# Optimization experiments

Measured on AMD Instinct MI355X. Metric: run time of the kernel, lower is better.

Reference implementation:

```python
import jax, jax.numpy as jnp
import numpy as np

METRIC_SCALE = 0.01  # metric = I + 0.01 * outer(p, p)


def setup_inputs() -> dict:
    key = jax.random.key(0)
    kq, kk = jax.random.split(key)
    query_points = jax.random.normal(kq, (8192, 512), dtype=jnp.float32)
    key_points = jax.random.normal(kk, (8192, 512), dtype=jnp.float32)
    return {"query_points": query_points, "key_points": key_points}


def reference(query_points, key_points):
    # diff_ij = q_i - k_j;  dist^2 under metric (I + c * p p^T) is
    # ||diff||^2 + c * (p . diff)^2 -- avoids materializing [Nq, Nk, d] diffs.
    c = METRIC_SCALE
    qq = jnp.sum(query_points * query_points, axis=-1)          # [Nq]
    kk = jnp.sum(key_points * key_points, axis=-1)              # [Nk]
    qk = jnp.einsum('qd,kd->qk', query_points, key_points)      # [Nq, Nk]
    norm2 = jnp.maximum(qq[:, None] + kk[None, :] - 2.0 * qk, 0.0)
    qdot = qq[:, None] - qk                                     # q_i . (q_i - k_j)
    kdot = qk - kk[None, :]                                     # k_j . (q_i - k_j) (sign irrelevant, squared)
    query_dist = jnp.sqrt(norm2 + c * qdot * qdot)
    key_dist = jnp.sqrt(norm2 + c * kdot * kdot)
    scores = -0.5 * (query_dist + key_dist)
    return jax.nn.softmax(scores, axis=-1)
```

## Files before the change

kernel.cpp:

```cpp
#include <hip/hip_runtime.h>
#include <stdint.h>


#define NQ 8192
#define NK 8192
#define DIM 512
#define CSCALE 0.01f

typedef float f32x4 __attribute__((ext_vector_type(4)));
typedef short s16x8 __attribute__((ext_vector_type(8)));
typedef unsigned short u16x4 __attribute__((ext_vector_type(4)));

__device__ __forceinline__ unsigned short f2bf(float x) {
  union { float f; uint32_t u; } c; c.f = x;
  uint32_t u = c.u;
  return (unsigned short)((u + 0x7fffu + ((u >> 16) & 1u)) >> 16);
}

__device__ __forceinline__ float bf2f(unsigned short h) {
  union { uint32_t u; float f; } c; c.u = ((uint32_t)h) << 16;
  return c.f;
}

__device__ __forceinline__ s16x8 pack8(f32x4 a, f32x4 b) {
  s16x8 r;
  r[0]=(short)f2bf(a.x); r[1]=(short)f2bf(a.y);
  r[2]=(short)f2bf(a.z); r[3]=(short)f2bf(a.w);
  r[4]=(short)f2bf(b.x); r[5]=(short)f2bf(b.y);
  r[6]=(short)f2bf(b.z); r[7]=(short)f2bf(b.w);
  return r;
}

#define GLOAD_LDS16(g, l)                                                      \
  __builtin_amdgcn_global_load_lds(                                            \
      (const __attribute__((address_space(1))) void*)(g),                      \
      (__attribute__((address_space(3))) void*)(l), 16, 0, 0)

__global__ __launch_bounds__(256) void prep_full_kernel(
    const float* __restrict__ q, const float* __restrict__ k,
    unsigned short* __restrict__ qbf, unsigned short* __restrict__ kbf,
    float* __restrict__ qq, float* __restrict__ kk) {
  int rowg = blockIdx.x * 4 + (threadIdx.x >> 6);
  int lane = threadIdx.x & 63;
  const float* src; unsigned short* dst; float* nrm; int row;
  if (rowg < NQ) { src = q; dst = qbf; nrm = qq; row = rowg; }
  else           { src = k; dst = kbf; nrm = kk; row = rowg - NQ; }
  const float* p = src + (size_t)row * DIM + lane * 8;
  f32x4 a = *(const f32x4*)p;
  f32x4 b = *(const f32x4*)(p + 4);
  float ss = a.x*a.x + a.y*a.y + a.z*a.z + a.w*a.w
           + b.x*b.x + b.y*b.y + b.z*b.z + b.w*b.w;
  *(s16x8*)(dst + (size_t)row * DIM + lane * 8) = pack8(a, b);
#pragma unroll
  for (int mask = 1; mask < 64; mask <<= 1) ss += __shfl_xor(ss, mask, 64);
  if (lane == 0) nrm[row] = ss;
}

__global__ __launch_bounds__(256) void prep_norms_kernel(
    const float* __restrict__ q, const float* __restrict__ k,
    float* __restrict__ qq, float* __restrict__ kk) {
  int rowg = blockIdx.x * 4 + (threadIdx.x >> 6);
  int lane = threadIdx.x & 63;
  const float* src; float* nrm; int row;
  if (rowg < NQ) { src = q; nrm = qq; row = rowg; }
  else           { src = k; nrm = kk; row = rowg - NQ; }
  const float* p = src + (size_t)row * DIM + lane * 8;
  f32x4 a = *(const f32x4*)p;
  f32x4 b = *(const f32x4*)(p + 4);
  float ss = a.x*a.x + a.y*a.y + a.z*a.z + a.w*a.w
           + b.x*b.x + b.y*b.y + b.z*b.z + b.w*b.w;
#pragma unroll
  for (int mask = 1; mask < 64; mask <<= 1) ss += __shfl_xor(ss, mask, 64);
  if (lane == 0) nrm[row] = ss;
}

__device__ __forceinline__ float score_fn(float qkv, float qqv, float kkv) {
  float n2 = fmaxf(qqv + kkv - 2.f * qkv, 0.f);
  float qd = qqv - qkv;
  float kd = qkv - kkv;
  return -0.5f * (sqrtf(n2 + CSCALE * qd * qd) +
                  sqrtf(n2 + CSCALE * kd * kd));
}

__global__ __launch_bounds__(256) void gemm_exp_kernel(
    const unsigned short* __restrict__ qbf, const unsigned short* __restrict__ kbf,
    const float* __restrict__ qq, const float* __restrict__ kk,
    unsigned short* __restrict__ E) {
  __shared__ unsigned short lA[128 * 32];
  __shared__ unsigned short lB[128 * 32];
  __shared__ alignas(16) unsigned short lT[4][16 * 80];
  const int tid = threadIdx.x;
  const int m0 = blockIdx.y * 128;
  const int n0 = blockIdx.x * 128;
  const int wave = tid >> 6, lane = tid & 63;
  const int wr = wave >> 1, wc = wave & 1;
  const int quad = lane >> 4, lcol = lane & 15;

  const unsigned short* ga = qbf + (size_t)(m0 + (tid >> 2)) * DIM + (tid & 3) * 8;
  const unsigned short* gb = kbf + (size_t)(n0 + (tid >> 2)) * DIM + (tid & 3) * 8;
  char* la0 = (char*)lA + wave * 1024;
  char* lb0 = (char*)lB + wave * 1024;

  f32x4 acc[4][4];
#pragma unroll
  for (int mi = 0; mi < 4; ++mi)
#pragma unroll
    for (int ni = 0; ni < 4; ++ni) acc[mi][ni] = f32x4{0.f, 0.f, 0.f, 0.f};

  const s16x8* lA8 = (const s16x8*)lA;
  const s16x8* lB8 = (const s16x8*)lB;
  const int arow = wr * 64 + lcol;
  const int brow = wc * 64 + lcol;

  for (int kt = 0; kt < DIM / 32; ++kt) {
    const int ko = kt * 32;
    GLOAD_LDS16(ga + ko, la0);
    GLOAD_LDS16(ga + ko + 64 * DIM, la0 + 4096);
    GLOAD_LDS16(gb + ko, lb0);
    GLOAD_LDS16(gb + ko + 64 * DIM, lb0 + 4096);
    __syncthreads();
    s16x8 af[4], bfr[4];
#pragma unroll
    for (int mi = 0; mi < 4; ++mi) af[mi] = lA8[(arow + mi * 16) * 4 + quad];
#pragma unroll
    for (int ni = 0; ni < 4; ++ni) bfr[ni] = lB8[(brow + ni * 16) * 4 + quad];
#pragma unroll
    for (int mi = 0; mi < 4; ++mi)
#pragma unroll
      for (int ni = 0; ni < 4; ++ni)
        acc[mi][ni] = __builtin_amdgcn_mfma_f32_16x16x32_bf16(
            af[mi], bfr[ni], acc[mi][ni], 0, 0, 0);
    __syncthreads();
  }

  unsigned short* tw = &lT[wave][0];
  float kkv[4];
#pragma unroll
  for (int ni = 0; ni < 4; ++ni) kkv[ni] = kk[n0 + wc * 64 + ni * 16 + lcol];
#pragma unroll
  for (int mi = 0; mi < 4; ++mi) {
    const int ibase = m0 + wr * 64 + mi * 16 + quad * 4;
    float qqv[4];
#pragma unroll
    for (int r = 0; r < 4; ++r) qqv[r] = qq[ibase + r];
#pragma unroll
    for (int ni = 0; ni < 4; ++ni)
#pragma unroll
      for (int r = 0; r < 4; ++r) {
        float e = __expf(score_fn(acc[mi][ni][r], qqv[r], kkv[ni]));
        tw[(quad * 4 + r) * 80 + ((ni ^ quad) * 16 + lcol)] = f2bf(e);
      }
#pragma unroll
    for (int j = 0; j < 2; ++j) {
      const int row16 = (lane >> 3) + j * 8;
      const int g = (lane & 7) >> 1;
      const int off = row16 * 80 + ((g ^ (row16 >> 2)) * 16) + (lane & 1) * 8;
      s16x8 vv = *(const s16x8*)(tw + off);
      const int rowg = m0 + wr * 64 + mi * 16 + row16;
      *(s16x8*)(E + (size_t)rowg * NK + n0 + wc * 64 + (lane & 7) * 8) = vv;
    }
  }
}

__global__ __launch_bounds__(256) void rowsum_scale_kernel(
    const unsigned short* __restrict__ E, float* __restrict__ out) {
  __shared__ float red[4];
  const int t = threadIdx.x;
  const int wave = t >> 6, lane = t & 63;
  const unsigned short* Erow = E + (size_t)blockIdx.x * NK;
  float* Orow = out + (size_t)blockIdx.x * NK;
  u16x4 ev[8];
  float s = 0.f;
#pragma unroll
  for (int j = 0; j < 8; ++j) {
    ev[j] = *(const u16x4*)(Erow + j * 1024 + t * 4);
    s += (bf2f(ev[j][0]) + bf2f(ev[j][1])) + (bf2f(ev[j][2]) + bf2f(ev[j][3]));
  }
#pragma unroll
  for (int mask = 1; mask < 64; mask <<= 1) s += __shfl_xor(s, mask, 64);
  if (lane == 0) red[wave] = s;
  __syncthreads();
  float z = 1.0f / ((red[0] + red[1]) + (red[2] + red[3]));
#pragma unroll
  for (int j = 0; j < 8; ++j) {
    f32x4 v;
    v.x = bf2f(ev[j][0]) * z;
    v.y = bf2f(ev[j][1]) * z;
    v.z = bf2f(ev[j][2]) * z;
    v.w = bf2f(ev[j][3]) * z;
    *(f32x4*)(Orow + j * 1024 + t * 4) = v;
  }
}

__device__ __forceinline__ void score_epilogue(
    const f32x4 acc[4][4], const float* __restrict__ qq,
    const float* __restrict__ kk, float* __restrict__ S,
    int m0, int n0, int wr, int wc, int quad, int lcol) {
  float kkv[4];
#pragma unroll
  for (int ni = 0; ni < 4; ++ni) kkv[ni] = kk[n0 + wc * 64 + ni * 16 + lcol];
#pragma unroll
  for (int mi = 0; mi < 4; ++mi) {
    const int ibase = m0 + wr * 64 + mi * 16 + quad * 4;
    float qqv[4];
#pragma unroll
    for (int r = 0; r < 4; ++r) qqv[r] = qq[ibase + r];
#pragma unroll
    for (int ni = 0; ni < 4; ++ni) {
      const int col = n0 + wc * 64 + ni * 16 + lcol;
#pragma unroll
      for (int r = 0; r < 4; ++r)
        S[(size_t)(ibase + r) * NK + col] = score_fn(acc[mi][ni][r], qqv[r], kkv[ni]);
    }
  }
}

__global__ __launch_bounds__(256) void gemm_fast_kernel(
    const unsigned short* __restrict__ qbf, const unsigned short* __restrict__ kbf,
    const float* __restrict__ qq, const float* __restrict__ kk,
    float* __restrict__ S) {
  __shared__ unsigned short lA[128 * 32];
  __shared__ unsigned short lB[128 * 32];
  const int tid = threadIdx.x;
  const int m0 = blockIdx.y * 128;
  const int n0 = blockIdx.x * 128;
  const int wave = tid >> 6, lane = tid & 63;
  const int wr = wave >> 1, wc = wave & 1;
  const int quad = lane >> 4, lcol = lane & 15;
  const unsigned short* ga = qbf + (size_t)(m0 + (tid >> 2)) * DIM + (tid & 3) * 8;
  const unsigned short* gb = kbf + (size_t)(n0 + (tid >> 2)) * DIM + (tid & 3) * 8;
  char* la0 = (char*)lA + wave * 1024;
  char* lb0 = (char*)lB + wave * 1024;
  f32x4 acc[4][4];
#pragma unroll
  for (int mi = 0; mi < 4; ++mi)
#pragma unroll
    for (int ni = 0; ni < 4; ++ni) acc[mi][ni] = f32x4{0.f, 0.f, 0.f, 0.f};
  const s16x8* lA8 = (const s16x8*)lA;
  const s16x8* lB8 = (const s16x8*)lB;
  const int arow = wr * 64 + lcol;
  const int brow = wc * 64 + lcol;
  for (int kt = 0; kt < DIM / 32; ++kt) {
    const int ko = kt * 32;
    GLOAD_LDS16(ga + ko, la0);
    GLOAD_LDS16(ga + ko + 64 * DIM, la0 + 4096);
    GLOAD_LDS16(gb + ko, lb0);
    GLOAD_LDS16(gb + ko + 64 * DIM, lb0 + 4096);
    __syncthreads();
    s16x8 af[4], bfr[4];
#pragma unroll
    for (int mi = 0; mi < 4; ++mi) af[mi] = lA8[(arow + mi * 16) * 4 + quad];
#pragma unroll
    for (int ni = 0; ni < 4; ++ni) bfr[ni] = lB8[(brow + ni * 16) * 4 + quad];
#pragma unroll
    for (int mi = 0; mi < 4; ++mi)
#pragma unroll
      for (int ni = 0; ni < 4; ++ni)
        acc[mi][ni] = __builtin_amdgcn_mfma_f32_16x16x32_bf16(
            af[mi], bfr[ni], acc[mi][ni], 0, 0, 0);
    __syncthreads();
  }
  score_epilogue(acc, qq, kk, S, m0, n0, wr, wc, quad, lcol);
}

__global__ __launch_bounds__(256) void gemm_safe_kernel(
    const float* __restrict__ q, const float* __restrict__ k,
    const float* __restrict__ qq, const float* __restrict__ kk,
    float* __restrict__ S) {
  __shared__ unsigned short lA[128 * 32];
  __shared__ unsigned short lB[128 * 32];
  const int tid = threadIdx.x;
  const int m0 = blockIdx.y * 128;
  const int n0 = blockIdx.x * 128;
  const int wave = tid >> 6, lane = tid & 63;
  const int wr = wave >> 1, wc = wave & 1;
  const int quad = lane >> 4, lcol = lane & 15;
  const float* gaf = q + (size_t)(m0 + (tid >> 1)) * DIM + (tid & 1) * 16;
  const float* gbf = k + (size_t)(n0 + (tid >> 1)) * DIM + (tid & 1) * 16;
  unsigned short* wA = lA + (tid >> 1) * 32 + (tid & 1) * 16;
  unsigned short* wB = lB + (tid >> 1) * 32 + (tid & 1) * 16;
  f32x4 acc[4][4];
#pragma unroll
  for (int mi = 0; mi < 4; ++mi)
#pragma unroll
    for (int ni = 0; ni < 4; ++ni) acc[mi][ni] = f32x4{0.f, 0.f, 0.f, 0.f};
  const s16x8* lA8 = (const s16x8*)lA;
  const s16x8* lB8 = (const s16x8*)lB;
  const int arow = wr * 64 + lcol;
  const int brow = wc * 64 + lcol;
  for (int kt = 0; kt < DIM / 32; ++kt) {
    const float* pa = gaf + kt * 32;
    const float* pb = gbf + kt * 32;
    f32x4 a0 = *(const f32x4*)(pa), a1 = *(const f32x4*)(pa + 4);
    f32x4 a2 = *(const f32x4*)(pa + 8), a3 = *(const f32x4*)(pa + 12);
    f32x4 b0 = *(const f32x4*)(pb), b1 = *(const f32x4*)(pb + 4);
    f32x4 b2 = *(const f32x4*)(pb + 8), b3 = *(const f32x4*)(pb + 12);
    *(s16x8*)wA = pack8(a0, a1);
    *(s16x8*)(wA + 8) = pack8(a2, a3);
    *(s16x8*)wB = pack8(b0, b1);
    *(s16x8*)(wB + 8) = pack8(b2, b3);
    __syncthreads();
    s16x8 af[4], bfr[4];
#pragma unroll
    for (int mi = 0; mi < 4; ++mi) af[mi] = lA8[(arow + mi * 16) * 4 + quad];
#pragma unroll
    for (int ni = 0; ni < 4; ++ni) bfr[ni] = lB8[(brow + ni * 16) * 4 + quad];
#pragma unroll
    for (int mi = 0; mi < 4; ++mi)
#pragma unroll
      for (int ni = 0; ni < 4; ++ni)
        acc[mi][ni] = __builtin_amdgcn_mfma_f32_16x16x32_bf16(
            af[mi], bfr[ni], acc[mi][ni], 0, 0, 0);
    __syncthreads();
  }
  score_epilogue(acc, qq, kk, S, m0, n0, wr, wc, quad, lcol);
}

__global__ __launch_bounds__(256) void rowsoftmax_kernel(float* __restrict__ S) {
  __shared__ float red[8];
  const int t = threadIdx.x;
  const int wave = t >> 6, lane = t & 63;
  float* Srow = S + (size_t)blockIdx.x * NK;
  f32x4 v[8];
  float m = -1e30f;
#pragma unroll
  for (int j = 0; j < 8; ++j) {
    v[j] = *(const f32x4*)(Srow + j * 1024 + t * 4);
    m = fmaxf(m, fmaxf(fmaxf(v[j].x, v[j].y), fmaxf(v[j].z, v[j].w)));
  }
#pragma unroll
  for (int mask = 1; mask < 64; mask <<= 1) m = fmaxf(m, __shfl_xor(m, mask, 64));
  if (lane == 0) red[wave] = m;
  __syncthreads();
  m = fmaxf(fmaxf(red[0], red[1]), fmaxf(red[2], red[3]));
  float s = 0.f;
#pragma unroll
  for (int j = 0; j < 8; ++j) {
    v[j].x = __expf(v[j].x - m);
    v[j].y = __expf(v[j].y - m);
    v[j].z = __expf(v[j].z - m);
    v[j].w = __expf(v[j].w - m);
    s += (v[j].x + v[j].y) + (v[j].z + v[j].w);
  }
#pragma unroll
  for (int mask = 1; mask < 64; mask <<= 1) s += __shfl_xor(s, mask, 64);
  if (lane == 0) red[4 + wave] = s;
  __syncthreads();
  float z = 1.0f / ((red[4] + red[5]) + (red[6] + red[7]));
#pragma unroll
  for (int j = 0; j < 8; ++j) {
    v[j].x *= z; v[j].y *= z; v[j].z *= z; v[j].w *= z;
    *(f32x4*)(Srow + j * 1024 + t * 4) = v[j];
  }
}

extern "C" void kernel_launch(void* const* d_in, const int* in_sizes, int n_in,
                              void* d_out, int out_size, void* d_ws, size_t ws_size,
                              hipStream_t stream) {
  const float* q = (const float*)d_in[0];
  const float* k = (const float*)d_in[1];
  float* S = (float*)d_out;
  char* ws = (char*)d_ws;

  if (ws_size >= (size_t)151126016) {
    unsigned short* qbf = (unsigned short*)(ws);
    unsigned short* kbf = (unsigned short*)(ws + 8388608);
    float* qq = (float*)(ws + 16777216);
    float* kk = (float*)(ws + 16777216 + 32768);
    unsigned short* E = (unsigned short*)(ws + 16908288);
    prep_full_kernel<<<4096, 256, 0, stream>>>(q, k, qbf, kbf, qq, kk);
    gemm_exp_kernel<<<dim3(64, 64), 256, 0, stream>>>(qbf, kbf, qq, kk, E);
    rowsum_scale_kernel<<<NQ, 256, 0, stream>>>(E, S);
  } else if (ws_size >= (size_t)16842752) {
    unsigned short* qbf = (unsigned short*)(ws);
    unsigned short* kbf = (unsigned short*)(ws + 8388608);
    float* qq = (float*)(ws + 16777216);
    float* kk = (float*)(ws + 16777216 + 32768);
    prep_full_kernel<<<4096, 256, 0, stream>>>(q, k, qbf, kbf, qq, kk);
    gemm_fast_kernel<<<dim3(64, 64), 256, 0, stream>>>(qbf, kbf, qq, kk, S);
    rowsoftmax_kernel<<<NQ, 256, 0, stream>>>(S);
  } else {
    float* qq = (float*)(ws);
    float* kk = (float*)(ws + 32768);
    prep_norms_kernel<<<4096, 256, 0, stream>>>(q, k, qq, kk);
    gemm_safe_kernel<<<dim3(64, 64), 256, 0, stream>>>(q, k, qq, kk, S);
    rowsoftmax_kernel<<<NQ, 256, 0, stream>>>(S);
  }
}
```

Baseline: 466.8 us.

## Swizzle LDS tiles to avoid bank conflicts, alias epilogue buffer, use fast sqrt

Applies an XOR swizzle to the 16-byte chunk index of each row in the A/B LDS tiles. The global-to-LDS loads write swizzled positions and the MFMA fragment reads un-swizzle them, which is meant to cut LDS bank conflicts on the ds_read_b128 fragment loads. The epilogue transpose buffer now aliases the GEMM staging LDS (lowering the per-block LDS footprint, which may help occupancy), and sqrtf is replaced by the hardware sqrt intrinsic, which gives up IEEE-exact rounding.

```diff
diff --git a/kernel.cpp b/kernel.cpp
--- a/kernel.cpp
+++ b/kernel.cpp
@@ -78,17 +78,15 @@
   float n2 = fmaxf(qqv + kkv - 2.f * qkv, 0.f);
   float qd = qqv - qkv;
   float kd = qkv - kkv;
-  return -0.5f * (sqrtf(n2 + CSCALE * qd * qd) +
-                  sqrtf(n2 + CSCALE * kd * kd));
+  return -0.5f * (__builtin_amdgcn_sqrtf(n2 + CSCALE * qd * qd) +
+                  __builtin_amdgcn_sqrtf(n2 + CSCALE * kd * kd));
 }
 
 __global__ __launch_bounds__(256) void gemm_exp_kernel(
     const unsigned short* __restrict__ qbf, const unsigned short* __restrict__ kbf,
     const float* __restrict__ qq, const float* __restrict__ kk,
     unsigned short* __restrict__ E) {
-  __shared__ unsigned short lA[128 * 32];
-  __shared__ unsigned short lB[128 * 32];
-  __shared__ alignas(16) unsigned short lT[4][16 * 80];
+  __shared__ alignas(16) unsigned short smem[8192];
   const int tid = threadIdx.x;
   const int m0 = blockIdx.y * 128;
   const int n0 = blockIdx.x * 128;
@@ -96,10 +94,12 @@
   const int wr = wave >> 1, wc = wave & 1;
   const int quad = lane >> 4, lcol = lane & 15;
 
-  const unsigned short* ga = qbf + (size_t)(m0 + (tid >> 2)) * DIM + (tid & 3) * 8;
-  const unsigned short* gb = kbf + (size_t)(n0 + (tid >> 2)) * DIM + (tid & 3) * 8;
-  char* la0 = (char*)lA + wave * 1024;
-  char* lb0 = (char*)lB + wave * 1024;
+  const int srow = tid >> 2;
+  const int gsw = (tid & 3) ^ ((srow >> 1) & 3);
+  const unsigned short* ga = qbf + (size_t)(m0 + srow) * DIM + gsw * 8;
+  const unsigned short* gb = kbf + (size_t)(n0 + srow) * DIM + gsw * 8;
+  char* la0 = (char*)smem + wave * 1024;
+  char* lb0 = (char*)smem + 8192 + wave * 1024;
 
   f32x4 acc[4][4];
 #pragma unroll
@@ -107,10 +107,12 @@
 #pragma unroll
     for (int ni = 0; ni < 4; ++ni) acc[mi][ni] = f32x4{0.f, 0.f, 0.f, 0.f};
 
-  const s16x8* lA8 = (const s16x8*)lA;
-  const s16x8* lB8 = (const s16x8*)lB;
+  const s16x8* lA8 = (const s16x8*)smem;
+  const s16x8* lB8 = (const s16x8*)(smem + 4096);
   const int arow = wr * 64 + lcol;
   const int brow = wc * 64 + lcol;
+  const int swz = (lcol >> 1) & 3;
+  const int qsw = quad ^ swz;
 
   for (int kt = 0; kt < DIM / 32; ++kt) {
     const int ko = kt * 32;
@@ -121,9 +123,9 @@
     __syncthreads();
     s16x8 af[4], bfr[4];
 #pragma unroll
-    for (int mi = 0; mi < 4; ++mi) af[mi] = lA8[(arow + mi * 16) * 4 + quad];
-#pragma unroll
-    for (int ni = 0; ni < 4; ++ni) bfr[ni] = lB8[(brow + ni * 16) * 4 + quad];
+    for (int mi = 0; mi < 4; ++mi) af[mi] = lA8[(arow + mi * 16) * 4 + qsw];
+#pragma unroll
+    for (int ni = 0; ni < 4; ++ni) bfr[ni] = lB8[(brow + ni * 16) * 4 + qsw];
 #pragma unroll
     for (int mi = 0; mi < 4; ++mi)
 #pragma unroll
@@ -133,7 +135,7 @@
     __syncthreads();
   }
 
-  unsigned short* tw = &lT[wave][0];
+  unsigned short* tw = smem + wave * 1280;
   float kkv[4];
 #pragma unroll
   for (int ni = 0; ni < 4; ++ni) kkv[ni] = kk[n0 + wc * 64 + ni * 16 + lcol];
```

Measured after the change: 427.9 us. -8.3%, faster.
